# Kernel optimization log

Hardware: AMD Instinct MI355X
Metric: run time of the kernel (lower is better)

## Reference

```python
import jax, jax.numpy as jnp
import numpy as np

D_MODEL = 2048
SLOTS = 8
D_FIELD = 256  # SLOTS * D_FIELD == proj output dim == 2048
BATCH = 2
SEQ = 4096


def setup_inputs() -> dict:
    key = jax.random.key(0)
    k1, k2 = jax.random.split(key, 2)
    x = jax.random.normal(k1, (BATCH, SEQ, D_MODEL), dtype=jnp.float32)
    # nn.Linear(d_model, slots*d_field): weight [out, in], bias [out]
    W = jax.random.normal(k2, (SLOTS * D_FIELD, D_MODEL), dtype=jnp.float32) * (1.0 / np.sqrt(D_MODEL))
    b = jnp.zeros((SLOTS * D_FIELD,), dtype=jnp.float32)
    horizons = jnp.array([1., 2., 4., 8., 16., 32., 64., 128.], dtype=jnp.float32)
    alphas = jnp.exp(-1.0 / horizons)  # per-slot EMA decay, length SLOTS
    return {"x": x, "W": W, "b": b, "alphas": alphas}


def reference(x, W, b, alphas):
    B, S, _ = x.shape
    # projection: [B,S,d_model] @ [d_model, slots*d_field] -> [B,S,slots,d_field]
    updates = (jnp.einsum('bsd,od->bso', x, W) + b).reshape(B, S, SLOTS, D_FIELD)
    # linear recurrence state_t = alpha * state_{t-1} + u_t, state_0 = 0,
    # via log-depth associative scan with elements (a_t, u_t)
    a = jnp.broadcast_to(alphas[None, None, :, None], updates.shape)

    def combine(c1, c2):
        a1, u1 = c1
        a2, u2 = c2
        return (a1 * a2, a2 * u1 + u2)

    _, state = jax.lax.associative_scan(combine, (a, updates), axis=1)
    return state  # [B,S,slots,d_field]
```

## Files before the change

kernel.cpp:

```cpp
#include <hip/hip_runtime.h>
#include <hip/hip_bf16.h>
#include <stdint.h>
#include <stddef.h>

#define D_MODEL 2048
#define NOUT    2048
#define BATCH   2
#define SEQ     4096
#define M_TOTAL (BATCH*SEQ)
#define SLOTS   8
#define D_FIELD 256
#define CHUNK   32
#define NCHUNK  (SEQ/CHUNK)
#define NWAVEC  64

typedef __attribute__((ext_vector_type(4))) float  floatx4;
typedef __attribute__((ext_vector_type(8))) __bf16 bf16x8;
typedef __attribute__((ext_vector_type(4))) __bf16 bf16x4;

__device__ __forceinline__ void async_copy16(const void* gsrc, void* ldst) {
  __builtin_amdgcn_global_load_lds(
      (__attribute__((address_space(1))) const void*)(uintptr_t)gsrc,
      (__attribute__((address_space(3))) void*)(uintptr_t)ldst,
      16, 0, 0);
}

__global__ void cast_kernel(const float* __restrict__ x,
                            const float* __restrict__ W,
                            __bf16* __restrict__ xb,
                            __bf16* __restrict__ wb,
                            int* __restrict__ ctr) {
  if (blockIdx.x == 0 && threadIdx.x < 8)
    __hip_atomic_store(&ctr[threadIdx.x], 0, __ATOMIC_RELAXED, __HIP_MEMORY_SCOPE_AGENT);
  const long long nx = (long long)M_TOTAL * D_MODEL;
  const long long nw = (long long)NOUT * D_MODEL;
  long long base = ((long long)blockIdx.x * blockDim.x + threadIdx.x) * 4;
  if (base < nx) {
    float4 v = *(const float4*)(x + base);
    bf16x4 o;
    o[0] = (__bf16)v.x; o[1] = (__bf16)v.y; o[2] = (__bf16)v.z; o[3] = (__bf16)v.w;
    *(bf16x4*)(xb + base) = o;
  } else {
    long long j = base - nx;
    if (j < nw) {
      float4 v = *(const float4*)(W + j);
      bf16x4 o;
      o[0] = (__bf16)v.x; o[1] = (__bf16)v.y; o[2] = (__bf16)v.z; o[3] = (__bf16)v.w;
      *(bf16x4*)(wb + j) = o;
    }
  }
}

#define VMW6 asm volatile("s_waitcnt vmcnt(6)" ::: "memory")
#define VMW4 asm volatile("s_waitcnt vmcnt(4)" ::: "memory")
#define VMW2 asm volatile("s_waitcnt vmcnt(2)" ::: "memory")
#define VMW0 asm volatile("s_waitcnt vmcnt(0)" ::: "memory")
#define LGKM0 do{ asm volatile("s_waitcnt lgkmcnt(0)" ::: "memory"); \
                  __builtin_amdgcn_sched_barrier(0); }while(0)
#define BAR do{ __builtin_amdgcn_s_barrier(); __builtin_amdgcn_sched_barrier(0); }while(0)

#define DSRD(off) (*(const bf16x8*)(smem + (off)))

#define STG(GP, ROFF, DSTOFF, KTN) do{ \
  async_copy16((GP) + (ROFF) + (KTN)*64,      smem + (DSTOFF)); \
  async_copy16((GP) + (ROFF) + (KTN)*64 + 32, smem + (DSTOFF) + 1024); }while(0)

#define RD_AF(BUF, MOFF) do{ \
  _Pragma("unroll") for (int i_ = 0; i_ < 4; ++i_){ \
  _Pragma("unroll") for (int k_ = 0; k_ < 2; ++k_){ \
    afr[i_][k_] = DSRD((BUF)*32768 + ((wM8+(MOFF)+i_)*2+k_)*1024 + fragOff); }} }while(0)

#define RD_BF(BUF, NOFF, DST) do{ \
  _Pragma("unroll") for (int j_ = 0; j_ < 2; ++j_){ \
  _Pragma("unroll") for (int k_ = 0; k_ < 2; ++k_){ \
    DST[j_][k_] = DSRD(65536 + (BUF)*32768 + ((wN4+(NOFF)+j_)*2+k_)*1024 + fragOff); }} }while(0)

#define MFMA_Q(AM, AN, BFR) do{ \
  __builtin_amdgcn_s_setprio(1); \
  _Pragma("unroll") for (int i_ = 0; i_ < 4; ++i_){ \
  _Pragma("unroll") for (int j_ = 0; j_ < 2; ++j_){ \
  _Pragma("unroll") for (int k_ = 0; k_ < 2; ++k_){ \
    acc[(AM)+i_][(AN)+j_] = __builtin_amdgcn_mfma_f32_16x16x32_bf16( \
        afr[i_][k_], BFR[j_][k_], acc[(AM)+i_][(AN)+j_], 0, 0, 0); }}} \
  __builtin_amdgcn_s_setprio(0); }while(0)

#define KTILE(BUF, TN1, TN2, MODE) do{ \
   \
  RD_AF(BUF, 0); \
  RD_BF(BUF, 0, bfr0); \
  if ((MODE) >= 1) { STG(gB, rB0, ((BUF)^1)*32768 + dB0, TN1); VMW6; } \
  else             { VMW2; } \
  BAR; LGKM0; \
  MFMA_Q(0, 0, bfr0); \
   \
  RD_BF(BUF, 2, bfr1); \
  if ((MODE) >= 1) { STG(gB, rB1, ((BUF)^1)*32768 + dB1, TN1); VMW6; } \
  else             { VMW0; } \
  BAR; LGKM0; \
  MFMA_Q(0, 2, bfr1); \
   \
  RD_AF(BUF, 4); \
  if ((MODE) >= 1) STG(gA, rA1, ((BUF)^1)*32768 + dA1, TN1); \
  BAR; LGKM0; \
  MFMA_Q(4, 2, bfr1); \
   \
  if ((MODE) == 2)      { STG(gA, rA0, (BUF)*32768 + dA0, TN2); VMW6; } \
  else if ((MODE) == 1) { VMW4; } \
  BAR; \
  MFMA_Q(4, 0, bfr0); \
}while(0)

#define CARRY_LD(P) __hip_atomic_load((P), __ATOMIC_RELAXED, __HIP_MEMORY_SCOPE_AGENT)

__global__ __launch_bounds__(512, 2) void gemm_scan_kernel(
    const __bf16* __restrict__ A,
    const __bf16* __restrict__ Bw,
    const float*  __restrict__ bias,
    const float*  __restrict__ alphas,
    float* __restrict__ C,
    float* __restrict__ wc,
    int*   __restrict__ ctr) {
  extern __shared__ __align__(16) char smem[];
  const int t    = threadIdx.x;
  const int lane = t & 63;
  const int w    = t >> 6;
  const int wM   = w >> 2;
  const int wN   = w & 3;
  const int m0   = blockIdx.x * 256;
  const int n0   = blockIdx.y * 256;

  const int lq = lane >> 4, lr = lane & 15;
  const int fragOff = (lr*64 + lq*16) ^ (((lr >> 3) & 1) << 5);
  const int wM8 = wM*8, wN4 = wN*4;

  const int lrow = lane >> 2;
  const int lcol = ((lane & 3) * 8) ^ ((lane >> 5) * 16);
  const int srA0 = (w & 3) + ((w >> 2) << 3), srA1 = srA0 + 4;
  const int srB0 = (w & 1) + ((w >> 1) << 2), srB1 = srB0 + 2;
  const __bf16* gA = A  + (size_t)m0 * D_MODEL + lcol;
  const __bf16* gB = Bw + (size_t)n0 * D_MODEL + lcol;
  const int rA0 = (srA0*16 + lrow) * D_MODEL;
  const int rA1 = (srA1*16 + lrow) * D_MODEL;
  const int rB0 = (srB0*16 + lrow) * D_MODEL;
  const int rB1 = (srB1*16 + lrow) * D_MODEL;
  const int dA0 = srA0*2048 + lane*16;
  const int dA1 = srA1*2048 + lane*16;
  const int dB0 = 65536 + srB0*2048 + lane*16;
  const int dB1 = 65536 + srB1*2048 + lane*16;

  floatx4 acc[8][4] = {};
  bf16x8 afr[4][2], bfr0[2][2], bfr1[2][2];

  STG(gA, rA0, dA0, 0);
  STG(gB, rB0, dB0, 0);
  STG(gB, rB1, dB1, 0);
  STG(gA, rA1, dA1, 0);
  STG(gA, rA0, 32768 + dA0, 1);
  VMW6;
  BAR;

#pragma unroll 1
  for (int p = 0; p < 15; ++p) {
    KTILE(0, 2*p+1, 2*p+2, 2);
    KTILE(1, 2*p+2, 2*p+3, 2);
  }
  KTILE(0, 31, 0, 1);
  KTILE(1, 0, 0, 0);

  const int mW0 = m0 + wM*128;
  const int nW0 = n0 + wN*64;
  const float alpha = alphas[nW0 >> 8];
  const float a2 = alpha*alpha, a4 = a2*a2, a8 = a4*a4, a16 = a8*a8, a32 = a16*a16;
  const float a64 = a32*a32, a128 = a64*a64;
  const float a256 = a128*a128, a512 = a256*a256, a1024 = a512*a512;
  float aq = 1.f;
#pragma unroll
  for (int i = 0; i < 3; ++i) if (i < 3 - lq) aq *= a4;
  float a4p = 1.f;
#pragma unroll
  for (int i = 0; i < 3; ++i) if (i < lq) a4p *= a4;
  const int bb  = mW0 >> 12;
  const int j0w = (mW0 & (SEQ - 1)) >> 5;
  const int jw  = j0w >> 2;
  float* wcb = wc + (size_t)bb * NWAVEC * NOUT;

  float bvv[4], tmv[4][8], rcl[4][4];
#pragma unroll
  for (int nf = 0; nf < 4; ++nf) {
    const int n = nW0 + nf*16 + lr;
    bvv[nf] = bias[n];
    const float bv = bvv[nf];
#pragma unroll
    for (int mf = 0; mf < 8; ++mf) {
      const floatx4 av = acc[mf][nf];
      tmv[nf][mf] = (((av[0]+bv)*alpha + (av[1]+bv))*alpha + (av[2]+bv))*alpha + (av[3]+bv);
    }
#pragma unroll
    for (int c = 0; c < 4; ++c) {
      float s = (tmv[nf][2*c]*a16 + tmv[nf][2*c+1]) * aq;
      s += __shfl_xor(s, 16, 64);
      s += __shfl_xor(s, 32, 64);
      rcl[nf][c] = s;
    }
    const float Wv = ((rcl[nf][0]*a32 + rcl[nf][1])*a32 + rcl[nf][2])*a32 + rcl[nf][3];
    if (lq == 0)
      __hip_atomic_store(&wcb[(size_t)jw*NOUT + n], Wv,
                         __ATOMIC_RELAXED, __HIP_MEMORY_SCOPE_AGENT);
  }

  __syncthreads();
  if (t == 0) {
    __hip_atomic_fetch_add(&ctr[blockIdx.y], 1, __ATOMIC_ACQ_REL, __HIP_MEMORY_SCOPE_AGENT);
    while (__hip_atomic_load(&ctr[blockIdx.y], __ATOMIC_ACQUIRE, __HIP_MEMORY_SCOPE_AGENT) < 32)
      __builtin_amdgcn_s_sleep(2);
  }
  __syncthreads();

  {
    const float* wcl = wcb + (nW0 + lq*16 + lr);
    float H = 0.f;
    int jp = 0;
    for (; jp + 8 <= jw; jp += 8) {
      float v[8];
#pragma unroll
      for (int i = 0; i < 8; ++i)
        v[i] = CARRY_LD(&wcl[(size_t)(jp + i)*NOUT]);
      float h = v[0];
#pragma unroll
      for (int i = 1; i < 8; ++i) h = h*a128 + v[i];
      H = H*a1024 + h;
    }
    for (; jp < jw; ++jp)
      H = H*a128 + CARRY_LD(&wcl[(size_t)jp*NOUT]);

    float s0[4];
#pragma unroll
    for (int nf = 0; nf < 4; ++nf) s0[nf] = __shfl(H, nf*16 + lr, 64);

#pragma unroll
    for (int nf = 0; nf < 4; ++nf) {
      const int n = nW0 + nf*16 + lr;
      const float bv = bvv[nf];
      float sp = s0[nf];
#pragma unroll
      for (int c = 0; c < 4; ++c) {
        if (c > 0)
          sp = a32*sp + rcl[nf][c-1];
        float ulo[4], uhi[4];
#pragma unroll
        for (int i = 0; i < 4; ++i) {
          ulo[i] = acc[2*c][nf][i]   + bv;
          uhi[i] = acc[2*c+1][nf][i] + bv;
        }
        const float Tlo = tmv[nf][2*c];
        const float Thi = tmv[nf][2*c+1];
        const float t0  = __shfl(Tlo, lr,      64);
        const float t1  = __shfl(Tlo, 16 + lr, 64);
        const float t2  = __shfl(Tlo, 32 + lr, 64);
        const float t3  = __shfl(Tlo, 48 + lr, 64);
        const float th0 = __shfl(Thi, lr,      64);
        const float th1 = __shfl(Thi, 16 + lr, 64);
        const float th2 = __shfl(Thi, 32 + lr, 64);
        float h = 0.f;
        if (lq > 0) h = t0;
        if (lq > 1) h = h*a4 + t1;
        if (lq > 2) h = h*a4 + t2;
        float Slo = a4p*sp + h;
        const float smid = (((t0*a4 + t1)*a4 + t2)*a4 + t3) + a16*sp;
        float hh = 0.f;
        if (lq > 0) hh = th0;
        if (lq > 1) hh = hh*a4 + th1;
        if (lq > 2) hh = hh*a4 + th2;
        float Shi = a4p*smid + hh;
        const size_t rowb = (size_t)(mW0 + 2*c*16 + lq*4);
        float s = Slo;
#pragma unroll
        for (int i = 0; i < 4; ++i) { s = alpha*s + ulo[i]; C[(rowb + i)*NOUT + n] = s; }
        s = Shi;
#pragma unroll
        for (int i = 0; i < 4; ++i) { s = alpha*s + uhi[i]; C[(rowb + 16 + i)*NOUT + n] = s; }
      }
    }
  }
}

extern "C" void kernel_launch(void* const* d_in, const int* in_sizes, int n_in,
                              void* d_out, int out_size, void* d_ws, size_t ws_size,
                              hipStream_t stream) {
  const float* x      = (const float*)d_in[0];
  const float* W      = (const float*)d_in[1];
  const float* bias   = (const float*)d_in[2];
  const float* alphas = (const float*)d_in[3];
  float* out = (float*)d_out;

  __bf16* xb = (__bf16*)d_ws;
  __bf16* wb = (__bf16*)((char*)d_ws + (size_t)M_TOTAL * D_MODEL * 2);
  float* wc  = (float*)((char*)d_ws + (size_t)M_TOTAL * D_MODEL * 2
                                     + (size_t)NOUT * D_MODEL * 2);
  int* ctr   = (int*)((char*)d_ws + (size_t)M_TOTAL * D_MODEL * 2
                                   + (size_t)NOUT * D_MODEL * 2
                                   + (size_t)BATCH * NWAVEC * NOUT * 4);

  {
    const long long total = ((long long)M_TOTAL * D_MODEL + (long long)NOUT * D_MODEL) / 4;
    const int blocks = (int)((total + 255) / 256);
    cast_kernel<<<blocks, 256, 0, stream>>>(x, W, xb, wb, ctr);
  }
  {
    dim3 grid(M_TOTAL / 256, NOUT / 256);
    gemm_scan_kernel<<<grid, 512, 131072, stream>>>(xb, wb, bias, alphas, out, wc, ctr);
  }
}
```

Baseline: 199.7 us.

## Software-pipeline LDS fragment reads across k-tiles and drop lgkmcnt waits

Restructures the GEMM main loop so the LDS fragment reads for the next k-tile (A low half and B first half) are issued during the current tile's MFMA phases. It uses double register sets (aflo/afhi, even/odd bfr0), removes the explicit lgkmcnt(0) waits, and reorders the global-to-LDS staging to match. The goal is to hide LDS read latency behind MFMA work. In exchange the kernel needs more fragment registers, which is a risk at 2 waves/SIMD occupancy with 512 threads, and it depends on compiler-inserted waits being correct.

```diff
diff --git a/kernel.cpp b/kernel.cpp
--- a/kernel.cpp
+++ b/kernel.cpp
@@ -55,8 +55,6 @@
 #define VMW4 asm volatile("s_waitcnt vmcnt(4)" ::: "memory")
 #define VMW2 asm volatile("s_waitcnt vmcnt(2)" ::: "memory")
 #define VMW0 asm volatile("s_waitcnt vmcnt(0)" ::: "memory")
-#define LGKM0 do{ asm volatile("s_waitcnt lgkmcnt(0)" ::: "memory"); \
-                  __builtin_amdgcn_sched_barrier(0); }while(0)
 #define BAR do{ __builtin_amdgcn_s_barrier(); __builtin_amdgcn_sched_barrier(0); }while(0)
 
 #define DSRD(off) (*(const bf16x8*)(smem + (off)))
@@ -65,49 +63,74 @@
   async_copy16((GP) + (ROFF) + (KTN)*64,      smem + (DSTOFF)); \
   async_copy16((GP) + (ROFF) + (KTN)*64 + 32, smem + (DSTOFF) + 1024); }while(0)
 
-#define RD_AF(BUF, MOFF) do{ \
+#define RD_A(BUF, MOFF, DST) do{ \
   _Pragma("unroll") for (int i_ = 0; i_ < 4; ++i_){ \
   _Pragma("unroll") for (int k_ = 0; k_ < 2; ++k_){ \
-    afr[i_][k_] = DSRD((BUF)*32768 + ((wM8+(MOFF)+i_)*2+k_)*1024 + fragOff); }} }while(0)
-
-#define RD_BF(BUF, NOFF, DST) do{ \
+    DST[i_][k_] = DSRD((BUF)*32768 + ((wM8+(MOFF)+i_)*2+k_)*1024 + fragOff); }} }while(0)
+
+#define RD_B(BUF, NOFF, DST) do{ \
   _Pragma("unroll") for (int j_ = 0; j_ < 2; ++j_){ \
   _Pragma("unroll") for (int k_ = 0; k_ < 2; ++k_){ \
     DST[j_][k_] = DSRD(65536 + (BUF)*32768 + ((wN4+(NOFF)+j_)*2+k_)*1024 + fragOff); }} }while(0)
 
-#define MFMA_Q(AM, AN, BFR) do{ \
+#define MFMA_Q(AM, AN, AF, BF) do{ \
   __builtin_amdgcn_s_setprio(1); \
   _Pragma("unroll") for (int i_ = 0; i_ < 4; ++i_){ \
   _Pragma("unroll") for (int j_ = 0; j_ < 2; ++j_){ \
   _Pragma("unroll") for (int k_ = 0; k_ < 2; ++k_){ \
     acc[(AM)+i_][(AN)+j_] = __builtin_amdgcn_mfma_f32_16x16x32_bf16( \
-        afr[i_][k_], BFR[j_][k_], acc[(AM)+i_][(AN)+j_], 0, 0, 0); }}} \
+        AF[i_][k_], BF[j_][k_], acc[(AM)+i_][(AN)+j_], 0, 0, 0); }}} \
   __builtin_amdgcn_s_setprio(0); }while(0)
 
-#define KTILE(BUF, TN1, TN2, MODE) do{ \
+#define KTILE_F(BUF, T1, T2, BC, BN) do{ \
    \
-  RD_AF(BUF, 0); \
-  RD_BF(BUF, 0, bfr0); \
-  if ((MODE) >= 1) { STG(gB, rB0, ((BUF)^1)*32768 + dB0, TN1); VMW6; } \
-  else             { VMW2; } \
-  BAR; LGKM0; \
-  MFMA_Q(0, 0, bfr0); \
+  RD_B(BUF, 2, bfr1); \
+  STG(gB, rB1, ((BUF)^1)*32768 + dB1, T1); \
+  VMW6; BAR; \
+  MFMA_Q(0, 0, aflo, BC); \
    \
-  RD_BF(BUF, 2, bfr1); \
-  if ((MODE) >= 1) { STG(gB, rB1, ((BUF)^1)*32768 + dB1, TN1); VMW6; } \
-  else             { VMW0; } \
-  BAR; LGKM0; \
-  MFMA_Q(0, 2, bfr1); \
+  RD_A(BUF, 4, afhi); \
+  STG(gA, rA1, ((BUF)^1)*32768 + dA1, T1); \
+  VMW4; BAR; \
+  MFMA_Q(0, 2, aflo, bfr1); \
    \
-  RD_AF(BUF, 4); \
-  if ((MODE) >= 1) STG(gA, rA1, ((BUF)^1)*32768 + dA1, TN1); \
-  BAR; LGKM0; \
-  MFMA_Q(4, 2, bfr1); \
+  RD_B((BUF)^1, 0, BN); \
+  STG(gA, rA0, (BUF)*32768 + dA0, T2); \
+  BAR; \
+  MFMA_Q(4, 2, afhi, bfr1); \
    \
-  if ((MODE) == 2)      { STG(gA, rA0, (BUF)*32768 + dA0, TN2); VMW6; } \
-  else if ((MODE) == 1) { VMW4; } \
+  RD_A((BUF)^1, 0, aflo); \
+  STG(gB, rB0, (BUF)*32768 + dB0, T2); \
+  VMW6; BAR; \
+  MFMA_Q(4, 0, afhi, BC); \
+}while(0)
+
+#define KTILE_T30(BUF, T1, BC, BN) do{ \
+  RD_B(BUF, 2, bfr1); \
+  STG(gB, rB1, ((BUF)^1)*32768 + dB1, T1); \
+  VMW6; BAR; \
+  MFMA_Q(0, 0, aflo, BC); \
+  RD_A(BUF, 4, afhi); \
+  STG(gA, rA1, ((BUF)^1)*32768 + dA1, T1); \
+  VMW4; BAR; \
+  MFMA_Q(0, 2, aflo, bfr1); \
+  RD_B((BUF)^1, 0, BN); \
   BAR; \
-  MFMA_Q(4, 0, bfr0); \
+  MFMA_Q(4, 2, afhi, bfr1); \
+  RD_A((BUF)^1, 0, aflo); \
+  VMW2; BAR; \
+  MFMA_Q(4, 0, afhi, BC); \
+}while(0)
+
+#define KTILE_T31(BUF, BC) do{ \
+  RD_B(BUF, 2, bfr1); \
+  VMW0; BAR; \
+  MFMA_Q(0, 0, aflo, BC); \
+  RD_A(BUF, 4, afhi); \
+  BAR; \
+  MFMA_Q(0, 2, aflo, bfr1); \
+  MFMA_Q(4, 2, afhi, bfr1); \
+  MFMA_Q(4, 0, afhi, BC); \
 }while(0)
 
 #define CARRY_LD(P) __hip_atomic_load((P), __ATOMIC_RELAXED, __HIP_MEMORY_SCOPE_AGENT)
@@ -149,23 +172,26 @@
   const int dB1 = 65536 + srB1*2048 + lane*16;
 
   floatx4 acc[8][4] = {};
-  bf16x8 afr[4][2], bfr0[2][2], bfr1[2][2];
-
+  bf16x8 aflo[4][2], afhi[4][2], bfr1[2][2], bfr0_e[2][2], bfr0_o[2][2];
+
+  STG(gB, rB1, dB1, 0);
   STG(gA, rA0, dA0, 0);
   STG(gB, rB0, dB0, 0);
-  STG(gB, rB1, dB1, 0);
   STG(gA, rA1, dA1, 0);
   STG(gA, rA0, 32768 + dA0, 1);
+  STG(gB, rB0, 32768 + dB0, 1);
   VMW6;
   BAR;
+  RD_A(0, 0, aflo);
+  RD_B(0, 0, bfr0_e);
 
 #pragma unroll 1
   for (int p = 0; p < 15; ++p) {
-    KTILE(0, 2*p+1, 2*p+2, 2);
-    KTILE(1, 2*p+2, 2*p+3, 2);
-  }
-  KTILE(0, 31, 0, 1);
-  KTILE(1, 0, 0, 0);
+    KTILE_F(0, 2*p+1, 2*p+2, bfr0_e, bfr0_o);
+    KTILE_F(1, 2*p+2, 2*p+3, bfr0_o, bfr0_e);
+  }
+  KTILE_T30(0, 31, bfr0_e, bfr0_o);
+  KTILE_T31(1, bfr0_o);
 
   const int mW0 = m0 + wM*128;
   const int nW0 = n0 + wN*64;
```

New measurement: 303.2 us. 1.52x slower.

## Restructure GEMM k-loop prefetch schedule with extra barriers around MFMA quadrants

Applied to the files above, without the earlier changes.

Reorders the global-to-LDS async copies within each k-tile so that B tiles for the next-next tile are prefetched earlier. Both B halves are now preloaded in the prologue, and the loop has dedicated tail variants for the last two tiles. Barriers are added after every MFMA quadrant, and the sched_barrier is dropped from BAR. The aim is deeper prefetch of B and less vmcnt stalling, at the cost of more workgroup barriers per tile.

```diff
diff --git a/kernel.cpp b/kernel.cpp
--- a/kernel.cpp
+++ b/kernel.cpp
@@ -52,12 +52,10 @@
 }
 
 #define VMW6 asm volatile("s_waitcnt vmcnt(6)" ::: "memory")
-#define VMW4 asm volatile("s_waitcnt vmcnt(4)" ::: "memory")
-#define VMW2 asm volatile("s_waitcnt vmcnt(2)" ::: "memory")
 #define VMW0 asm volatile("s_waitcnt vmcnt(0)" ::: "memory")
 #define LGKM0 do{ asm volatile("s_waitcnt lgkmcnt(0)" ::: "memory"); \
                   __builtin_amdgcn_sched_barrier(0); }while(0)
-#define BAR do{ __builtin_amdgcn_s_barrier(); __builtin_amdgcn_sched_barrier(0); }while(0)
+#define BAR  __builtin_amdgcn_s_barrier()
 
 #define DSRD(off) (*(const bf16x8*)(smem + (off)))
 
@@ -84,29 +82,68 @@
         afr[i_][k_], BFR[j_][k_], acc[(AM)+i_][(AN)+j_], 0, 0, 0); }}} \
   __builtin_amdgcn_s_setprio(0); }while(0)
 
-#define KTILE(BUF, TN1, TN2, MODE) do{ \
+#define KTILE_F(BUF, TN1, TN2) do{ \
    \
   RD_AF(BUF, 0); \
   RD_BF(BUF, 0, bfr0); \
-  if ((MODE) >= 1) { STG(gB, rB0, ((BUF)^1)*32768 + dB0, TN1); VMW6; } \
-  else             { VMW2; } \
+  STG(gA, rA1, ((BUF)^1)*32768 + dA1, TN1); \
   BAR; LGKM0; \
   MFMA_Q(0, 0, bfr0); \
+  BAR; \
    \
   RD_BF(BUF, 2, bfr1); \
-  if ((MODE) >= 1) { STG(gB, rB1, ((BUF)^1)*32768 + dB1, TN1); VMW6; } \
-  else             { VMW0; } \
+  STG(gA, rA0, (BUF)*32768 + dA0, TN2); \
   BAR; LGKM0; \
   MFMA_Q(0, 2, bfr1); \
+  BAR; \
    \
   RD_AF(BUF, 4); \
-  if ((MODE) >= 1) STG(gA, rA1, ((BUF)^1)*32768 + dA1, TN1); \
+  STG(gB, rB0, (BUF)*32768 + dB0, TN2); \
   BAR; LGKM0; \
   MFMA_Q(4, 2, bfr1); \
+  BAR; \
    \
-  if ((MODE) == 2)      { STG(gA, rA0, (BUF)*32768 + dA0, TN2); VMW6; } \
-  else if ((MODE) == 1) { VMW4; } \
-  BAR; \
+  STG(gB, rB1, (BUF)*32768 + dB1, TN2); \
+  VMW6; \
+  BAR; \
+  MFMA_Q(4, 0, bfr0); \
+  BAR; \
+}while(0)
+
+#define KTILE_T30(BUF, TN1) do{ \
+  RD_AF(BUF, 0); \
+  RD_BF(BUF, 0, bfr0); \
+  STG(gA, rA1, ((BUF)^1)*32768 + dA1, TN1); \
+  BAR; LGKM0; \
+  MFMA_Q(0, 0, bfr0); \
+  BAR; \
+  RD_BF(BUF, 2, bfr1); \
+  BAR; LGKM0; \
+  MFMA_Q(0, 2, bfr1); \
+  BAR; \
+  RD_AF(BUF, 4); \
+  BAR; LGKM0; \
+  MFMA_Q(4, 2, bfr1); \
+  BAR; \
+  VMW0; \
+  BAR; \
+  MFMA_Q(4, 0, bfr0); \
+  BAR; \
+}while(0)
+
+#define KTILE_T31(BUF) do{ \
+  RD_AF(BUF, 0); \
+  RD_BF(BUF, 0, bfr0); \
+  BAR; LGKM0; \
+  MFMA_Q(0, 0, bfr0); \
+  BAR; \
+  RD_BF(BUF, 2, bfr1); \
+  BAR; LGKM0; \
+  MFMA_Q(0, 2, bfr1); \
+  BAR; \
+  RD_AF(BUF, 4); \
+  BAR; LGKM0; \
+  MFMA_Q(4, 2, bfr1); \
   MFMA_Q(4, 0, bfr0); \
 }while(0)
 
@@ -156,16 +193,18 @@
   STG(gB, rB1, dB1, 0);
   STG(gA, rA1, dA1, 0);
   STG(gA, rA0, 32768 + dA0, 1);
+  STG(gB, rB0, 32768 + dB0, 1);
+  STG(gB, rB1, 32768 + dB1, 1);
   VMW6;
   BAR;
 
 #pragma unroll 1
   for (int p = 0; p < 15; ++p) {
-    KTILE(0, 2*p+1, 2*p+2, 2);
-    KTILE(1, 2*p+2, 2*p+3, 2);
-  }
-  KTILE(0, 31, 0, 1);
-  KTILE(1, 0, 0, 0);
+    KTILE_F(0, 2*p+1, 2*p+2);
+    KTILE_F(1, 2*p+2, 2*p+3);
+  }
+  KTILE_T30(0, 31);
+  KTILE_T31(1);
 
   const int mW0 = m0 + wM*128;
   const int nW0 = n0 + wN*64;
```

Measured after the change: 201.9 us. Within noise of the previous version (+1.1%).
